# Optimization experiments

Hardware: AMD Instinct MI355X
Metric: run time of the kernel (lower is better)

The kernel has to match this reference:

```python
import jax, jax.numpy as jnp
import numpy as np

N = 50000      # nodes
E = 800000     # edges (before self-loops)
G = 256        # graphs in batch
IN = 64        # in_dim
H = 8          # n_heads
C = 16         # gat_dim (per-head out channels)
HID = 128      # decoder hidden
OUT = H * C    # 128 = concat GAT output = graph_embedding_dim
NEG_SLOPE = 0.2


def setup_inputs() -> dict:
    key = jax.random.key(0)
    ks = jax.random.split(key, 12)
    op_features = jax.random.normal(ks[0], (N, IN), dtype=jnp.float32)
    edge_index = jax.random.randint(ks[1], (2, E), 0, N, dtype=jnp.int64)
    batch_index = jnp.sort(jax.random.randint(ks[2], (N,), 0, G, dtype=jnp.int64))
    # GATConv params (PyG: lin weight, att_src, att_dst, bias)
    W_gat = jax.random.normal(ks[3], (IN, H * C), dtype=jnp.float32) / np.sqrt(IN)
    att_src = jax.random.normal(ks[4], (H, C), dtype=jnp.float32) / np.sqrt(C)
    att_dst = jax.random.normal(ks[5], (H, C), dtype=jnp.float32) / np.sqrt(C)
    bias_gat = jnp.zeros((H * C,), dtype=jnp.float32)
    # Decoder MLP: Linear(OUT+OUT, 128) -> ReLU -> Linear(128, 1)
    W1 = jax.random.normal(ks[6], (2 * OUT, HID), dtype=jnp.float32) / np.sqrt(2 * OUT)
    b1 = jnp.zeros((HID,), dtype=jnp.float32)
    W2 = jax.random.normal(ks[7], (HID, 1), dtype=jnp.float32) / np.sqrt(HID)
    b2 = jnp.zeros((1,), dtype=jnp.float32)
    return {
        "op_features": op_features, "edge_index": edge_index, "batch_index": batch_index,
        "W_gat": W_gat, "att_src": att_src, "att_dst": att_dst, "bias_gat": bias_gat,
        "W1": W1, "b1": b1, "W2": W2, "b2": b2,
    }


def _gat_conv(x_in, src, dst, W_gat, att_src, att_dst, bias_gat):
    # x: [N, H, C] transformed node features
    x = (x_in @ W_gat).reshape(N, H, C)
    # per-node attention logits (PyG splits alpha into src+dst halves)
    a_src = jnp.einsum('nhc,hc->nh', x, att_src)   # [N, H]
    a_dst = jnp.einsum('nhc,hc->nh', x, att_dst)   # [N, H]
    # edge logits: message flows src -> dst
    alpha = jax.nn.leaky_relu(a_src[src] + a_dst[dst], NEG_SLOPE)  # [E', H]
    # scatter-softmax over incoming edges of each dst node
    m = jax.ops.segment_max(alpha, dst, num_segments=N)            # [N, H]
    e = jnp.exp(alpha - m[dst])                                    # [E', H]
    s = jax.ops.segment_sum(e, dst, num_segments=N)                # [N, H]
    a = e / s[dst]
    # weighted aggregation of source features
    out = jax.ops.segment_sum(a[:, :, None] * x[src], dst, num_segments=N)  # [N, H, C]
    return out.reshape(N, H * C) + bias_gat


def reference(op_features, edge_index, batch_index, W_gat, att_src, att_dst,
              bias_gat, W1, b1, W2, b2):
    # add self-loops (PyG GATConv default add_self_loops=True)
    loop = jnp.arange(N, dtype=edge_index.dtype)
    src = jnp.concatenate([edge_index[0], loop])
    dst = jnp.concatenate([edge_index[1], loop])

    op_embedding = jax.nn.elu(_gat_conv(op_features, src, dst,
                                        W_gat, att_src, att_dst, bias_gat))  # [N, OUT]
    # global_mean_pool
    sums = jax.ops.segment_sum(op_embedding, batch_index, num_segments=G)    # [G, OUT]
    cnts = jax.ops.segment_sum(jnp.ones((N,), op_embedding.dtype), batch_index, num_segments=G)
    graph_embedding = sums / jnp.maximum(cnts, 1.0)[:, None]
    # gather-broadcast + concat + MLP decoder
    combined = jnp.concatenate([op_embedding, graph_embedding[batch_index]], axis=1)  # [N, 2*OUT]
    h = jax.nn.relu(combined @ W1 + b1)
    scores = (h @ W2 + b2).squeeze(-1)   # [N]
    return scores, graph_embedding
```

## Files before the change

kernel.cpp:

```cpp
#include <hip/hip_runtime.h>
#include <hip/hip_bf16.h>
#include <hip/hip_fp16.h>

constexpr int N_   = 50000;
constexpr int E_   = 800000;
constexpr int G_   = 256;
constexpr int IN_  = 64;
constexpr int H_   = 8;
constexpr int OUT_ = 128;
constexpr float NEG_SLOPE = 0.2f;
constexpr int NBUCK = (N_ + 255) / 256;
constexpr int EPB   = 2048;
constexpr int NBINB = (E_ + EPB - 1) / EPB;
constexpr int CAP   = 6144;
constexpr int NXF   = (N_ + 63) / 64;

typedef _Float16 f16x8 __attribute__((ext_vector_type(8)));
typedef float    f32x4 __attribute__((ext_vector_type(4)));

constexpr size_t OFF_X      = 0;
constexpr size_t OFF_EMBH   = OFF_X      + (size_t)N_*OUT_*2;
constexpr size_t OFF_ASRC   = OFF_X      + (size_t)N_*OUT_*4;
constexpr size_t OFF_ADST   = OFF_ASRC   + (size_t)N_*H_*4;
constexpr size_t OFF_PAIRS  = OFF_ADST   + (size_t)N_*H_*4;
constexpr size_t OFF_BCNT   = OFF_PAIRS  + (size_t)NBUCK*CAP*4;
constexpr size_t OFF_WT     = OFF_BCNT   + 1024;
constexpr size_t OFF_WP     = OFF_WT     + 128*128*2;
constexpr size_t OFF_ROWS   = OFF_WP     + 18432;
constexpr size_t OFF_EIDX   = OFF_ROWS   + 200448;
constexpr size_t OFF_GPART  = OFF_EIDX   + (size_t)E_*4;
constexpr size_t OFF_GSUM   = OFF_GPART  + (size_t)G_*OUT_*4;

__global__ void k_prep(const float* __restrict__ Wg, const float* __restrict__ att_s,
                       const float* __restrict__ att_d, const float* __restrict__ W1,
                       __half* __restrict__ wp, __half* __restrict__ wt,
                       int* __restrict__ bcnt, float* __restrict__ gsum) {
    const int b = blockIdx.x, t = threadIdx.x;
    if (b == 0) {
        for (int i = t; i < NBUCK; i += 256) bcnt[i] = 0;
        for (int idx = t; idx < 16 * 64; idx += 256) {
            int jp = idx >> 6, k = idx & 63;
            int h = jp & 7;
            const float* att = (jp < 8) ? att_s : att_d;
            float s = 0.f;
#pragma unroll
            for (int c = 0; c < 16; ++c)
                s = fmaf(Wg[k * 128 + h * 16 + c], att[h * 16 + c], s);
            wp[(128 + jp) * 64 + k] = __float2half(s);
        }
    } else if (b <= 8) {
        for (int idx = t; idx < 1024; idx += 256) {
            int e = (b - 1) * 1024 + idx;
            int j = e >> 6, k = e & 63;
            wp[j * 64 + k] = __float2half(Wg[k * 128 + j]);
        }
    } else {
        for (int idx = t; idx < 2048; idx += 256) {
            int e = (b - 9) * 2048 + idx;
            int j = e >> 7, k = e & 127;
            wt[j * 128 + k] = __float2half(W1[(size_t)k * 128 + j]);
        }
        for (int idx = t; idx < 4096; idx += 256)
            gsum[(size_t)(b - 9) * 4096 + idx] = 0.f;
    }
}

__global__ __launch_bounds__(256) void k_binx(const int* __restrict__ src,
                                              const int* __restrict__ dst,
                                              int* __restrict__ bcnt,
                                              unsigned int* __restrict__ pairs,
                                              const float* __restrict__ feat,
                                              const __half* __restrict__ wp,
                                              __half* __restrict__ xh,
                                              float* __restrict__ asrc,
                                              float* __restrict__ adst) {
    union SMem {
        struct { int cnt[NBUCK]; int base[NBUCK]; } bin;
        struct { _Float16 fs[64][64]; _Float16 wp_s[144][64]; } xf;
    };
    __shared__ SMem sm;
    const int tid = threadIdx.x;

    if (blockIdx.x < NBINB) {
        int* cnt  = sm.bin.cnt;
        int* base = sm.bin.base;
        for (int i = tid; i < NBUCK; i += 256) cnt[i] = 0;
        __syncthreads();
        const int e0 = blockIdx.x * EPB;
        const int ne = min(EPB, E_ - e0);
        for (int i = tid; i < ne; i += 256) atomicAdd(&cnt[dst[e0 + i] >> 8], 1);
        __syncthreads();
        for (int i = tid; i < NBUCK; i += 256) {
            int c = cnt[i];
            base[i] = (c > 0) ? atomicAdd(&bcnt[i], c) : 0;
            cnt[i] = 0;
        }
        __syncthreads();
        for (int i = tid; i < ne; i += 256) {
            int d = dst[e0 + i];
            int s = src[e0 + i];
            int b = d >> 8;
            int p = base[b] + atomicAdd(&cnt[b], 1);
            pairs[(size_t)b * CAP + p] = ((unsigned int)(d & 255) << 16) | (unsigned int)s;
        }
        return;
    }

    const int base = (blockIdx.x - NBINB) * 64;
    for (int c = tid; c < 1152; c += 256) {
        int j = c >> 3, kk = (c & 7) * 8;
        *(float4*)&sm.xf.wp_s[j][kk] = *(const float4*)&wp[j * 64 + kk];
    }
    for (int c = tid; c < 512; c += 256) {
        int nl = c >> 3, kk = (c & 7) * 8;
        int n = base + nl;
        _Float16 h8[8];
        if (n < N_) {
            float4 f0 = *(const float4*)&feat[(size_t)n * 64 + kk];
            float4 f1 = *(const float4*)&feat[(size_t)n * 64 + kk + 4];
            h8[0]=(_Float16)f0.x; h8[1]=(_Float16)f0.y; h8[2]=(_Float16)f0.z; h8[3]=(_Float16)f0.w;
            h8[4]=(_Float16)f1.x; h8[5]=(_Float16)f1.y; h8[6]=(_Float16)f1.z; h8[7]=(_Float16)f1.w;
        } else {
#pragma unroll
            for (int q = 0; q < 8; ++q) h8[q] = (_Float16)0.f;
        }
        *(float4*)&sm.xf.fs[nl][kk] = *(float4*)h8;
    }
    __syncthreads();

    const int wv   = tid >> 6;
    const int lane = tid & 63;
    const int rc   = lane & 15;
    const int kh   = lane >> 4;

    f32x4 acc[9];
#pragma unroll
    for (int nt = 0; nt < 9; ++nt) acc[nt] = (f32x4){0.f, 0.f, 0.f, 0.f};

#pragma unroll
    for (int kt = 0; kt < 2; ++kt) {
        f16x8 a = *(const f16x8*)&sm.xf.fs[wv * 16 + rc][kt * 32 + kh * 8];
#pragma unroll
        for (int nt = 0; nt < 9; ++nt) {
            f16x8 bfr = *(const f16x8*)&sm.xf.wp_s[nt * 16 + rc][kt * 32 + kh * 8];
            acc[nt] = __builtin_amdgcn_mfma_f32_16x16x32_f16(a, bfr, acc[nt], 0, 0, 0);
        }
    }

#pragma unroll
    for (int r = 0; r < 4; ++r) {
        int n = base + wv * 16 + kh * 4 + r;
        if (n >= N_) continue;
#pragma unroll
        for (int nt = 0; nt < 8; ++nt)
            xh[(size_t)n * OUT_ + nt * 16 + rc] = __float2half(acc[nt][r]);
        if (rc < 8) asrc[n * H_ + rc] = acc[8][r];
        else        adst[n * H_ + (rc - 8)] = acc[8][r];
    }
}

__global__ __launch_bounds__(256) void k_scat3(const unsigned int* __restrict__ pairs,
                                               const int* __restrict__ bcnt,
                                               int* __restrict__ rowstart,
                                               int* __restrict__ eidx) {
    __shared__ int sh[256];
    __shared__ int h0[256];
    __shared__ int h1[256];
    __shared__ int cur[256];
    const int b    = blockIdx.x >> 1;
    const int half = blockIdx.x & 1;
    const int t    = threadIdx.x;

    int v0 = (t < NBUCK) ? bcnt[t] : 0;
    sh[t] = v0;
    __syncthreads();
    for (int off = 1; off < 256; off <<= 1) {
        int u = (t >= off) ? sh[t - off] : 0;
        __syncthreads();
        sh[t] += u;
        __syncthreads();
    }
    const int bstart_b = (b == 0) ? 0 : sh[b - 1];
    const int nb = bcnt[b];
    const int nh = nb >> 1;
    __syncthreads();

    h0[t] = 0;
    h1[t] = 0;
    __syncthreads();
    const size_t p0 = (size_t)b * CAP;
    for (int i = t; i < nh; i += 256) atomicAdd(&h0[pairs[p0 + i] >> 16], 1);
    for (int i = nh + t; i < nb; i += 256) atomicAdd(&h1[pairs[p0 + i] >> 16], 1);
    __syncthreads();
    int v = h0[t] + h1[t];
    sh[t] = v;
    __syncthreads();
    for (int off = 1; off < 256; off <<= 1) {
        int u = (t >= off) ? sh[t - off] : 0;
        __syncthreads();
        sh[t] += u;
        __syncthreads();
    }
    int rs = bstart_b + sh[t] - v;
    if (half == 0) {
        int n = b * 256 + t;
        if (n < N_) rowstart[n] = rs;
        if (b == NBUCK - 1 && t == 0) rowstart[N_] = E_;
    }
    cur[t] = rs + (half ? h0[t] : 0);
    __syncthreads();
    const int ibeg = half ? nh : 0;
    const int iend = half ? nb : nh;
    for (int i = ibeg + t; i < iend; i += 256) {
        unsigned int pk = pairs[p0 + i];
        int pos = atomicAdd(&cur[pk >> 16], 1);
        eidx[pos] = (int)(pk & 0xFFFFu);
    }
}

__global__ void k_agg(const int* __restrict__ rowstart, const int* __restrict__ eidx,
                      const __half* __restrict__ xh, const float* __restrict__ asrc,
                      const float* __restrict__ adst, const float* __restrict__ bias,
                      __half* __restrict__ embh) {
    const int dn   = blockIdx.x * 4 + (threadIdx.x >> 6);
    const int lane = threadIdx.x & 63;
    const int h    = lane >> 3;
    const float adst_h = adst[dn * H_ + h];
    const uint choff = (uint)lane * 2;

    const int beg = rowstart[dn];
    const int end = rowstart[dn + 1];

    float ax = 0.f, ay = 0.f, sw = 0.f;
    int i = beg;
    for (; i + 3 < end; i += 4) {
        int s0 = eidx[i];
        int s1 = eidx[i + 1];
        int s2 = eidx[i + 2];
        int s3 = eidx[i + 3];
        __half2 x0 = *(const __half2*)(xh + ((uint)s0 * OUT_ + choff));
        __half2 x1 = *(const __half2*)(xh + ((uint)s1 * OUT_ + choff));
        __half2 x2 = *(const __half2*)(xh + ((uint)s2 * OUT_ + choff));
        __half2 x3 = *(const __half2*)(xh + ((uint)s3 * OUT_ + choff));
        float a0 = asrc[(uint)s0 * H_ + h] + adst_h;
        float a1 = asrc[(uint)s1 * H_ + h] + adst_h;
        float a2 = asrc[(uint)s2 * H_ + h] + adst_h;
        float a3 = asrc[(uint)s3 * H_ + h] + adst_h;
        a0 = (a0 > 0.f) ? a0 : NEG_SLOPE * a0;
        a1 = (a1 > 0.f) ? a1 : NEG_SLOPE * a1;
        a2 = (a2 > 0.f) ? a2 : NEG_SLOPE * a2;
        a3 = (a3 > 0.f) ? a3 : NEG_SLOPE * a3;
        float w0 = __expf(a0);
        float w1 = __expf(a1);
        float w2 = __expf(a2);
        float w3 = __expf(a3);
        float2 f0 = __half22float2(x0);
        float2 f1 = __half22float2(x1);
        float2 f2 = __half22float2(x2);
        float2 f3 = __half22float2(x3);
        ax = fmaf(w0, f0.x, fmaf(w1, f1.x, fmaf(w2, f2.x, fmaf(w3, f3.x, ax))));
        ay = fmaf(w0, f0.y, fmaf(w1, f1.y, fmaf(w2, f2.y, fmaf(w3, f3.y, ay))));
        sw += (w0 + w1) + (w2 + w3);
    }
    for (; i < end; ++i) {
        int s0 = eidx[i];
        __half2 x0 = *(const __half2*)(xh + ((uint)s0 * OUT_ + choff));
        float a0 = asrc[(uint)s0 * H_ + h] + adst_h;
        a0 = (a0 > 0.f) ? a0 : NEG_SLOPE * a0;
        float w0 = __expf(a0);
        float2 f0 = __half22float2(x0);
        ax = fmaf(w0, f0.x, ax);
        ay = fmaf(w0, f0.y, ay);
        sw += w0;
    }
    {
        float al = asrc[(uint)dn * H_ + h] + adst_h;
        al = (al > 0.f) ? al : NEG_SLOPE * al;
        float w = __expf(al);
        __half2 xv = *(const __half2*)(xh + ((uint)dn * OUT_ + choff));
        float2 fv = __half22float2(xv);
        ax = fmaf(w, fv.x, ax);
        ay = fmaf(w, fv.y, ay);
        sw += w;
    }
    float ox = ax / sw + bias[lane * 2];
    float oy = ay / sw + bias[lane * 2 + 1];
    ox = (ox > 0.f) ? ox : expm1f(ox);
    oy = (oy > 0.f) ? oy : expm1f(oy);
    *(__half2*)&embh[(size_t)dn * OUT_ + lane * 2] = __floats2half2_rn(ox, oy);
}

__global__ void k_pool(const __half* __restrict__ embh, const int* __restrict__ batch,
                       float* __restrict__ gsum) {
    int c   = threadIdx.x & 63;
    int grp = threadIdx.x >> 6;
    int base = blockIdx.x * 64 + grp * 16;
    float rx = 0.f, ry = 0.f;
    int gcur = -1;
    for (int i = 0; i < 16; ++i) {
        int n = base + i;
        if (n >= N_) break;
        int g = batch[n];
        if (g != gcur) {
            if (gcur >= 0) {
                unsafeAtomicAdd(&gsum[gcur * OUT_ + 2 * c], rx);
                unsafeAtomicAdd(&gsum[gcur * OUT_ + 2 * c + 1], ry);
            }
            gcur = g; rx = ry = 0.f;
        }
        __half2 v = *(const __half2*)&embh[(size_t)n * OUT_ + 2 * c];
        float2 f = __half22float2(v);
        rx += f.x; ry += f.y;
    }
    if (gcur >= 0) {
        unsafeAtomicAdd(&gsum[gcur * OUT_ + 2 * c], rx);
        unsafeAtomicAdd(&gsum[gcur * OUT_ + 2 * c + 1], ry);
    }
}

__global__ void k_graph(const int* __restrict__ batch, const float* __restrict__ gsum,
                        const float* __restrict__ W1, const float* __restrict__ b1,
                        float* __restrict__ outg, float* __restrict__ gpart) {
    const int g = blockIdx.x;
    const int j = threadIdx.x;
    __shared__ float ge[128];
    __shared__ int cnt_s;
    if (j == 0) {
        int lo = 0, hi = N_;
        while (lo < hi) { int m = (lo + hi) >> 1; if (batch[m] < g) lo = m + 1; else hi = m; }
        int start = lo;
        lo = 0; hi = N_;
        while (lo < hi) { int m = (lo + hi) >> 1; if (batch[m] <= g) lo = m + 1; else hi = m; }
        cnt_s = lo - start;
    }
    __syncthreads();
    float v = gsum[g * 128 + j] / fmaxf((float)cnt_s, 1.f);
    ge[j] = v;
    outg[g * 128 + j] = v;
    __syncthreads();
    float s = b1[j];
    const float* w = W1 + (size_t)128 * 128 + j;
    for (int k = 0; k < 128; ++k) s = fmaf(ge[k], w[(size_t)k * 128], s);
    gpart[g * 128 + j] = s;
}

__global__ __launch_bounds__(256) void k_dec3(const __half* __restrict__ embh,
                                              const __half* __restrict__ wtg,
                                              const float* __restrict__ gpart,
                                              const int* __restrict__ batch,
                                              const float* __restrict__ W2,
                                              const float* __restrict__ b2,
                                              float* __restrict__ scores) {
    __shared__ _Float16 wt_s[128][128];
    __shared__ _Float16 emb_s[64][128];
    __shared__ float    w2_s[128];
    const int base = blockIdx.x * 64;
    const int tid  = threadIdx.x;

    for (int c = tid; c < 2048; c += 256) {
        int j = c >> 4, kk = (c & 15) * 8;
        *(float4*)&wt_s[j][kk] = *(const float4*)&wtg[j * 128 + kk];
    }
    for (int c = tid; c < 1024; c += 256) {
        int nl = c >> 4, kk = (c & 15) * 8;
        int n = base + nl;
        if (n < N_)
            *(float4*)&emb_s[nl][kk] = *(const float4*)&embh[(size_t)n * 128 + kk];
        else
            *(float4*)&emb_s[nl][kk] = make_float4(0.f, 0.f, 0.f, 0.f);
    }
    if (tid < 128) w2_s[tid] = W2[tid];
    __syncthreads();

    const int wv   = tid >> 6;
    const int lane = tid & 63;
    const int rc   = lane & 15;
    const int kh   = lane >> 4;

    f32x4 acc[8];
#pragma unroll
    for (int nt = 0; nt < 8; ++nt) acc[nt] = (f32x4){0.f, 0.f, 0.f, 0.f};

#pragma unroll
    for (int kt = 0; kt < 4; ++kt) {
        f16x8 a = *(const f16x8*)&emb_s[wv * 16 + rc][kt * 32 + kh * 8];
#pragma unroll
        for (int nt = 0; nt < 8; ++nt) {
            f16x8 bfr = *(const f16x8*)&wt_s[nt * 16 + rc][kt * 32 + kh * 8];
            acc[nt] = __builtin_amdgcn_mfma_f32_16x16x32_f16(a, bfr, acc[nt], 0, 0, 0);
        }
    }

    const float b2v = b2[0];
    float s[4] = {0.f, 0.f, 0.f, 0.f};
    int   gi[4];
#pragma unroll
    for (int r = 0; r < 4; ++r) {
        int n = base + wv * 16 + kh * 4 + r;
        gi[r] = (n < N_) ? batch[n] : 0;
    }
#pragma unroll
    for (int nt = 0; nt < 8; ++nt) {
        int j = nt * 16 + rc;
        float w2 = w2_s[j];
#pragma unroll
        for (int r = 0; r < 4; ++r) {
            float hv = acc[nt][r] + gpart[(size_t)gi[r] * 128 + j];
            hv = (hv > 0.f) ? hv : 0.f;
            s[r] = fmaf(hv, w2, s[r]);
        }
    }
#pragma unroll
    for (int r = 0; r < 4; ++r) {
#pragma unroll
        for (int m = 8; m >= 1; m >>= 1) s[r] += __shfl_xor(s[r], m, 16);
    }
    if (rc == 0) {
#pragma unroll
        for (int r = 0; r < 4; ++r) {
            int n = base + wv * 16 + kh * 4 + r;
            if (n < N_) scores[n] = s[r] + b2v;
        }
    }
}

extern "C" void kernel_launch(void* const* d_in, const int* in_sizes, int n_in,
                              void* d_out, int out_size, void* d_ws, size_t ws_size,
                              hipStream_t stream) {
    const float* feat   = (const float*)d_in[0];
    const int*   ei     = (const int*)d_in[1];
    const int*   batch  = (const int*)d_in[2];
    const float* Wg     = (const float*)d_in[3];
    const float* att_s  = (const float*)d_in[4];
    const float* att_d  = (const float*)d_in[5];
    const float* bias_g = (const float*)d_in[6];
    const float* W1     = (const float*)d_in[7];
    const float* b1     = (const float*)d_in[8];
    const float* W2     = (const float*)d_in[9];
    const float* b2     = (const float*)d_in[10];
    char*  wsb = (char*)d_ws;
    float* out = (float*)d_out;

    const int* src = ei;
    const int* dst = ei + E_;

    __half* XH    = (__half*)(wsb + OFF_X);
    __half* EMBH  = (__half*)(wsb + OFF_EMBH);
    float*  ASRC  = (float*)(wsb + OFF_ASRC);
    float*  ADST  = (float*)(wsb + OFF_ADST);
    unsigned int* PAIRS = (unsigned int*)(wsb + OFF_PAIRS);
    int*    BCNT  = (int*)  (wsb + OFF_BCNT);
    __half* WT    = (__half*)(wsb + OFF_WT);
    __half* WP    = (__half*)(wsb + OFF_WP);
    int*    ROWS  = (int*)  (wsb + OFF_ROWS);
    int*    EIDX  = (int*)  (wsb + OFF_EIDX);
    float*  GPART = (float*)(wsb + OFF_GPART);
    float*  GSUM  = (float*)(wsb + OFF_GSUM);

    k_prep<<<17, 256, 0, stream>>>(Wg, att_s, att_d, W1, WP, WT, BCNT, GSUM);
    k_binx<<<NBINB + NXF, 256, 0, stream>>>(src, dst, BCNT, PAIRS,
                                            feat, WP, XH, ASRC, ADST);
    k_scat3<<<2 * NBUCK, 256, 0, stream>>>(PAIRS, BCNT, ROWS, EIDX);
    k_agg<<<N_ / 4, 256, 0, stream>>>(ROWS, EIDX, XH, ASRC, ADST, bias_g, EMBH);
    k_pool<<<(N_ + 63) / 64, 256, 0, stream>>>(EMBH, batch, GSUM);
    k_graph<<<G_, 128, 0, stream>>>(batch, GSUM, W1, b1, out + N_, GPART);
    k_dec3<<<(N_ + 63) / 64, 256, 0, stream>>>(EMBH, WT, GPART, batch, W2, b2, out);
}
```

Measured before the change: 127.6 us.

## Fuse mean-pool accumulation into GAT aggregation and unroll edge loop by eight

Removes the separate pooling kernel by reducing the four node outputs of each aggregation block in shared memory and atomically adding them into per-graph sums. This saves a kernel launch and a re-read of the fp16 embeddings. It also adds an 8-way unrolled edge loop for more memory-level parallelism in the gather. In exchange, atomics per graph grow because only four nodes are combined per block, and the extra barrier adds contention on the graph-sum addresses.

```diff
diff --git a/kernel.cpp b/kernel.cpp
--- a/kernel.cpp
+++ b/kernel.cpp
@@ -221,8 +221,10 @@
 __global__ void k_agg(const int* __restrict__ rowstart, const int* __restrict__ eidx,
                       const __half* __restrict__ xh, const float* __restrict__ asrc,
                       const float* __restrict__ adst, const float* __restrict__ bias,
+                      const int* __restrict__ batch, float* __restrict__ gsum,
                       __half* __restrict__ embh) {
-    const int dn   = blockIdx.x * 4 + (threadIdx.x >> 6);
+    const int wvi  = threadIdx.x >> 6;
+    const int dn   = blockIdx.x * 4 + wvi;
     const int lane = threadIdx.x & 63;
     const int h    = lane >> 3;
     const float adst_h = adst[dn * H_ + h];
@@ -233,6 +235,61 @@
 
     float ax = 0.f, ay = 0.f, sw = 0.f;
     int i = beg;
+    for (; i + 7 < end; i += 8) {
+        int s0 = eidx[i];
+        int s1 = eidx[i + 1];
+        int s2 = eidx[i + 2];
+        int s3 = eidx[i + 3];
+        int s4 = eidx[i + 4];
+        int s5 = eidx[i + 5];
+        int s6 = eidx[i + 6];
+        int s7 = eidx[i + 7];
+        __half2 x0 = *(const __half2*)(xh + ((uint)s0 * OUT_ + choff));
+        __half2 x1 = *(const __half2*)(xh + ((uint)s1 * OUT_ + choff));
+        __half2 x2 = *(const __half2*)(xh + ((uint)s2 * OUT_ + choff));
+        __half2 x3 = *(const __half2*)(xh + ((uint)s3 * OUT_ + choff));
+        __half2 x4 = *(const __half2*)(xh + ((uint)s4 * OUT_ + choff));
+        __half2 x5 = *(const __half2*)(xh + ((uint)s5 * OUT_ + choff));
+        __half2 x6 = *(const __half2*)(xh + ((uint)s6 * OUT_ + choff));
+        __half2 x7 = *(const __half2*)(xh + ((uint)s7 * OUT_ + choff));
+        float a0 = asrc[(uint)s0 * H_ + h] + adst_h;
+        float a1 = asrc[(uint)s1 * H_ + h] + adst_h;
+        float a2 = asrc[(uint)s2 * H_ + h] + adst_h;
+        float a3 = asrc[(uint)s3 * H_ + h] + adst_h;
+        float a4 = asrc[(uint)s4 * H_ + h] + adst_h;
+        float a5 = asrc[(uint)s5 * H_ + h] + adst_h;
+        float a6 = asrc[(uint)s6 * H_ + h] + adst_h;
+        float a7 = asrc[(uint)s7 * H_ + h] + adst_h;
+        a0 = (a0 > 0.f) ? a0 : NEG_SLOPE * a0;
+        a1 = (a1 > 0.f) ? a1 : NEG_SLOPE * a1;
+        a2 = (a2 > 0.f) ? a2 : NEG_SLOPE * a2;
+        a3 = (a3 > 0.f) ? a3 : NEG_SLOPE * a3;
+        a4 = (a4 > 0.f) ? a4 : NEG_SLOPE * a4;
+        a5 = (a5 > 0.f) ? a5 : NEG_SLOPE * a5;
+        a6 = (a6 > 0.f) ? a6 : NEG_SLOPE * a6;
+        a7 = (a7 > 0.f) ? a7 : NEG_SLOPE * a7;
+        float w0 = __expf(a0);
+        float w1 = __expf(a1);
+        float w2 = __expf(a2);
+        float w3 = __expf(a3);
+        float w4 = __expf(a4);
+        float w5 = __expf(a5);
+        float w6 = __expf(a6);
+        float w7 = __expf(a7);
+        float2 f0 = __half22float2(x0);
+        float2 f1 = __half22float2(x1);
+        float2 f2 = __half22float2(x2);
+        float2 f3 = __half22float2(x3);
+        float2 f4 = __half22float2(x4);
+        float2 f5 = __half22float2(x5);
+        float2 f6 = __half22float2(x6);
+        float2 f7 = __half22float2(x7);
+        ax = fmaf(w0, f0.x, fmaf(w1, f1.x, fmaf(w2, f2.x, fmaf(w3, f3.x, ax))));
+        ax = fmaf(w4, f4.x, fmaf(w5, f5.x, fmaf(w6, f6.x, fmaf(w7, f7.x, ax))));
+        ay = fmaf(w0, f0.y, fmaf(w1, f1.y, fmaf(w2, f2.y, fmaf(w3, f3.y, ay))));
+        ay = fmaf(w4, f4.y, fmaf(w5, f5.y, fmaf(w6, f6.y, fmaf(w7, f7.y, ay))));
+        sw += ((w0 + w1) + (w2 + w3)) + ((w4 + w5) + (w6 + w7));
+    }
     for (; i + 3 < end; i += 4) {
         int s0 = eidx[i];
         int s1 = eidx[i + 1];
@@ -288,33 +345,32 @@
     ox = (ox > 0.f) ? ox : expm1f(ox);
     oy = (oy > 0.f) ? oy : expm1f(oy);
     *(__half2*)&embh[(size_t)dn * OUT_ + lane * 2] = __floats2half2_rn(ox, oy);
-}
-
-__global__ void k_pool(const __half* __restrict__ embh, const int* __restrict__ batch,
-                       float* __restrict__ gsum) {
-    int c   = threadIdx.x & 63;
-    int grp = threadIdx.x >> 6;
-    int base = blockIdx.x * 64 + grp * 16;
-    float rx = 0.f, ry = 0.f;
-    int gcur = -1;
-    for (int i = 0; i < 16; ++i) {
-        int n = base + i;
-        if (n >= N_) break;
-        int g = batch[n];
-        if (g != gcur) {
-            if (gcur >= 0) {
-                unsafeAtomicAdd(&gsum[gcur * OUT_ + 2 * c], rx);
-                unsafeAtomicAdd(&gsum[gcur * OUT_ + 2 * c + 1], ry);
+
+    __shared__ float px[4][64];
+    __shared__ float py[4][64];
+    __shared__ int   gidv[4];
+    px[wvi][lane] = ox;
+    py[wvi][lane] = oy;
+    if (lane == 0) gidv[wvi] = batch[dn];
+    __syncthreads();
+    if (wvi == 0) {
+        float sx = px[0][lane], sy = py[0][lane];
+        int gc = gidv[0];
+#pragma unroll
+        for (int w = 1; w < 4; ++w) {
+            if (gidv[w] == gc) {
+                sx += px[w][lane];
+                sy += py[w][lane];
+            } else {
+                unsafeAtomicAdd(&gsum[gc * OUT_ + lane * 2], sx);
+                unsafeAtomicAdd(&gsum[gc * OUT_ + lane * 2 + 1], sy);
+                gc = gidv[w];
+                sx = px[w][lane];
+                sy = py[w][lane];
             }
-            gcur = g; rx = ry = 0.f;
-        }
-        __half2 v = *(const __half2*)&embh[(size_t)n * OUT_ + 2 * c];
-        float2 f = __half22float2(v);
-        rx += f.x; ry += f.y;
-    }
-    if (gcur >= 0) {
-        unsafeAtomicAdd(&gsum[gcur * OUT_ + 2 * c], rx);
-        unsafeAtomicAdd(&gsum[gcur * OUT_ + 2 * c + 1], ry);
+        }
+        unsafeAtomicAdd(&gsum[gc * OUT_ + lane * 2], sx);
+        unsafeAtomicAdd(&gsum[gc * OUT_ + lane * 2 + 1], sy);
     }
 }
 
@@ -461,8 +517,8 @@
     k_binx<<<NBINB + NXF, 256, 0, stream>>>(src, dst, BCNT, PAIRS,
                                             feat, WP, XH, ASRC, ADST);
     k_scat3<<<2 * NBUCK, 256, 0, stream>>>(PAIRS, BCNT, ROWS, EIDX);
-    k_agg<<<N_ / 4, 256, 0, stream>>>(ROWS, EIDX, XH, ASRC, ADST, bias_g, EMBH);
-    k_pool<<<(N_ + 63) / 64, 256, 0, stream>>>(EMBH, batch, GSUM);
+    k_agg<<<N_ / 4, 256, 0, stream>>>(ROWS, EIDX, XH, ASRC, ADST, bias_g,
+                                      batch, GSUM, EMBH);
     k_graph<<<G_, 128, 0, stream>>>(batch, GSUM, W1, b1, out + N_, GPART);
     k_dec3<<<(N_ + 63) / 64, 256, 0, stream>>>(EMBH, WT, GPART, batch, W2, b2, out);
 }
```

Result: faster. 120.6 us (median of 2 runs) (-5.5%).
